# Performance work log

Measured on AMD Instinct MI355X. Metric: run time of the kernel, lower is better.

The kernel has to match this reference:

```python
import jax, jax.numpy as jnp
import numpy as np

BETA = 0.1
TRUNC = 1.0
MIN_VALID_RATIO = 0.3


def _wls_affine(x, y, w):
    # Weighted least squares fit of y ~ s*x + t over the last axis.
    sw = w.sum(-1)
    swx = (w * x).sum(-1)
    swy = (w * y).sum(-1)
    swxx = (w * x * x).sum(-1)
    swxy = (w * x * y).sum(-1)
    det = sw * swxx - swx * swx
    det = jnp.where(jnp.abs(det) < 1e-12, 1e-12, det)
    s = (sw * swxy - swx * swy) / det
    t = (swxx * swy - swx * swxy) / det
    return s, t


def _align_depth_affine(x, y, w, trunc):
    # Truncated robust affine alignment: initial WLS fit, then refit with
    # weights of points whose weighted residual exceeds `trunc` zeroed out
    # (falling back to the original weights if everything is truncated).
    s0, t0 = _wls_affine(x, y, w)
    e = w * jnp.abs(s0[..., None] * x + t0[..., None] - y)
    w2 = w * (e < trunc).astype(w.dtype)
    w2 = jnp.where(w2.sum(-1, keepdims=True) > 1e-8, w2, w)
    return _wls_affine(x, y, w2)


def _smooth(err, beta):
    if beta == 0:
        return err
    return jnp.where(err < beta, 0.5 * err * err / beta, err - 0.5 * beta)


def setup_inputs() -> dict:
    key = jax.random.key(0)
    k1, k2, k3 = jax.random.split(key, 3)
    B = 8
    P = 4096  # num_patches
    K = 256   # patch_pixel_count
    N = P * K
    pred_depth = jax.random.uniform(k1, (B, N), jnp.float32, 0.05, 5.0)
    gt_depth = jax.random.uniform(k2, (B, N), jnp.float32, 0.05, 5.0)
    mask = jax.random.bernoulli(k3, 0.8, (B, N))
    global_scale = jnp.ones((B,), jnp.float32)
    return {
        "pred_depth": pred_depth,
        "gt_depth": gt_depth,
        "mask": mask,
        "global_scale": global_scale,
        "num_patches": P,
        "patch_pixel_count": K,
    }


def reference(pred_depth, gt_depth, mask, global_scale, num_patches, patch_pixel_count):
    B = pred_depth.shape[0]
    P, K = num_patches, patch_pixel_count
    x = pred_depth.reshape(B, P, K)
    y = gt_depth.reshape(B, P, K)
    m = mask.reshape(B, P, K).astype(x.dtype)

    valid_ratio = m.mean(-1)                      # (B, P)
    msum = m.sum(-1)
    mean_depth = jnp.where(msum > 0, (y * m).sum(-1) / jnp.maximum(msum, 1.0), 1.0)

    w = m / jnp.maximum(y, 1e-5)                  # alignment weights (B, P, K)
    s, t = _align_depth_affine(x, y, w, TRUNC)    # (B, P) scale / shift per patch

    ratio = s / jnp.maximum(global_scale[:, None], 1e-12)
    gs_ok = jnp.where(global_scale[:, None] > 0, (ratio >= 0.1) & (ratio <= 10.0), True)
    valid = (valid_ratio >= MIN_VALID_RATIO) & (s > 0) & gs_ok  # (B, P)

    aligned = s[..., None] * x + t[..., None]
    pw = m / jnp.maximum(y, 0.1 * mean_depth[..., None])
    patch_loss = _smooth(jnp.abs(aligned - y) * pw, BETA).mean(-1)  # (B, P)

    vf = valid.astype(x.dtype)
    cnt = vf.sum()
    loss = jnp.where(cnt > 0, (patch_loss * vf).sum() / jnp.maximum(cnt, 1.0), 0.0)
    return loss
```

## Files before the change

### kernel.cpp

```cpp
#include <hip/hip_runtime.h>


#define WPB 4
#define NSLOTS 64
#define MAXBLK 2048

__device__ __forceinline__ float wredu(float v) {
#define DPP_ADD(ctrl)                                                        \
  v += __int_as_float(__builtin_amdgcn_update_dpp(                           \
      0, __float_as_int(v), (ctrl), 0xf, 0xf, true))
  DPP_ADD(0x111);
  DPP_ADD(0x112);
  DPP_ADD(0x114);
  DPP_ADD(0x118);
  DPP_ADD(0x142);
  DPP_ADD(0x143);
#undef DPP_ADD
  return __int_as_float(__builtin_amdgcn_readlane(__float_as_int(v), 63));
}

__device__ __forceinline__ float frcp(float x) {
  return __builtin_amdgcn_rcpf(x);
}

__global__ __launch_bounds__(256) void moge_patch_kernel(
    const float* __restrict__ xg,
    const float* __restrict__ yg,
    const int*   __restrict__ mg,
    const float* __restrict__ gsg,
    const int*   __restrict__ pP,
    const int*   __restrict__ pK,
    int B,
    float* __restrict__ ws,
    float* __restrict__ out) {
  const int P = pP[0];
  const int K = pK[0];
  const int lane = threadIdx.x & 63;
  const int wib  = threadIdx.x >> 6;
  const int total_patches = B * P;
  const int wave_stride = gridDim.x * WPB;
  const float invK = 1.0f / (float)K;

  if (K == 256) {
    int patch = blockIdx.x * WPB + wib;
    if (patch < total_patches) {
      const int loff = lane * 4;
      long base = (long)patch * 256 + loff;
      float4 x4 = *(const float4*)(xg + base);
      float4 y4 = *(const float4*)(yg + base);
      int4   m4 = *(const int4*)(mg + base);

      for (;;) {
        const int next = patch + wave_stride;
        const bool has_next = next < total_patches;
        const long nbase = (has_next ? (long)next * 256 : 0) + loff;
        const float4 nx4 = *(const float4*)(xg + nbase);
        const float4 ny4 = *(const float4*)(yg + nbase);
        const int4   nm4 = *(const int4*)(mg + nbase);

        float xr[4] = {x4.x, x4.y, x4.z, x4.w};
        float yr[4] = {y4.x, y4.y, y4.z, y4.w};
        float mr[4] = {m4.x ? 1.f : 0.f, m4.y ? 1.f : 0.f,
                       m4.z ? 1.f : 0.f, m4.w ? 1.f : 0.f};
        float wr[4];

        float sw = 0.f, swx = 0.f, swy = 0.f, swxx = 0.f, swxy = 0.f;
        float msum = 0.f, symsum = 0.f;
        #pragma unroll
        for (int i = 0; i < 4; ++i) {
          const float m = mr[i], xx = xr[i], yy = yr[i];
          const float w = m * frcp(fmaxf(yy, 1e-5f));
          wr[i] = w;
          const float wx = w * xx;
          sw += w; swx += wx; swy = fmaf(w, yy, swy);
          swxx = fmaf(wx, xx, swxx); swxy = fmaf(wx, yy, swxy);
          msum += m; symsum = fmaf(m, yy, symsum);
        }
        sw = wredu(sw); swx = wredu(swx); swy = wredu(swy);
        swxx = wredu(swxx); swxy = wredu(swxy);

        float det = sw * swxx - swx * swx;
        if (fabsf(det) < 1e-12f) det = 1e-12f;
        float rdet = frcp(det);
        const float s0 = (sw * swxy - swx * swy) * rdet;
        const float t0 = (swxx * swy - swx * swxy) * rdet;

        float sw2 = 0.f, swx2 = 0.f, swy2 = 0.f, swxx2 = 0.f, swxy2 = 0.f;
        #pragma unroll
        for (int i = 0; i < 4; ++i) {
          const float xx = xr[i], yy = yr[i], w = wr[i];
          const float e = w * fabsf(fmaf(s0, xx, t0) - yy);
          const float w2 = (e < 1.0f) ? w : 0.f;
          const float w2x = w2 * xx;
          sw2 += w2; swx2 += w2x; swy2 = fmaf(w2, yy, swy2);
          swxx2 = fmaf(w2x, xx, swxx2); swxy2 = fmaf(w2x, yy, swxy2);
        }
        sw2 = wredu(sw2); swx2 = wredu(swx2); swy2 = wredu(swy2);
        swxx2 = wredu(swxx2); swxy2 = wredu(swxy2);
        msum = wredu(msum); symsum = wredu(symsum);

        if (sw2 > 1e-8f) {
          sw = sw2; swx = swx2; swy = swy2; swxx = swxx2; swxy = swxy2;
        }
        det = sw * swxx - swx * swx;
        if (fabsf(det) < 1e-12f) det = 1e-12f;
        rdet = frcp(det);
        const float s = (sw * swxy - swx * swy) * rdet;
        const float t = (swxx * swy - swx * swxy) * rdet;

        const float mean_depth =
            (msum > 0.f) ? (symsum * frcp(fmaxf(msum, 1.f))) : 1.f;
        const float yfloor = 0.1f * mean_depth;

        float lsum = 0.f;
        #pragma unroll
        for (int i = 0; i < 4; ++i) {
          const float pw = mr[i] * frcp(fmaxf(yr[i], yfloor));
          const float err = fabsf(fmaf(s, xr[i], t) - yr[i]) * pw;
          lsum += (err < 0.1f) ? (5.0f * err * err) : (err - 0.05f);
        }
        const float patch_loss = wredu(lsum) * invK;

        const float gs = gsg[patch / P];
        const float ratio = s * frcp(fmaxf(gs, 1e-12f));
        const bool gs_ok = (gs > 0.f) ? (ratio >= 0.1f && ratio <= 10.0f) : true;
        const bool valid = (msum * invK >= 0.3f) && (s > 0.f) && gs_ok;

        if (lane == 0 && valid) {
          const int slot = patch & (NSLOTS - 1);
          atomicAdd(&ws[slot], patch_loss);
          atomicAdd(&ws[NSLOTS + slot], 1.0f);
        }

        if (!has_next) break;
        patch = next; x4 = nx4; y4 = ny4; m4 = nm4;
      }
    }
  } else {
    for (int patch = blockIdx.x * WPB + wib; patch < total_patches;
         patch += wave_stride) {
      const long base = (long)patch * (long)K;
      const float* xp = xg + base;
      const float* yp = yg + base;
      const int*   mp = mg + base;

      float sw = 0.f, swx = 0.f, swy = 0.f, swxx = 0.f, swxy = 0.f;
      float msum = 0.f, symsum = 0.f;
      for (int j = lane; j < K; j += 64) {
        const float m = mp[j] ? 1.f : 0.f;
        const float xx = xp[j], yy = yp[j];
        const float w = m * frcp(fmaxf(yy, 1e-5f));
        const float wx = w * xx;
        sw += w; swx += wx; swy = fmaf(w, yy, swy);
        swxx = fmaf(wx, xx, swxx); swxy = fmaf(wx, yy, swxy);
        msum += m; symsum = fmaf(m, yy, symsum);
      }
      sw = wredu(sw); swx = wredu(swx); swy = wredu(swy);
      swxx = wredu(swxx); swxy = wredu(swxy);
      msum = wredu(msum); symsum = wredu(symsum);

      float det = sw * swxx - swx * swx;
      if (fabsf(det) < 1e-12f) det = 1e-12f;
      float rdet = frcp(det);
      const float s0 = (sw * swxy - swx * swy) * rdet;
      const float t0 = (swxx * swy - swx * swxy) * rdet;

      float sw2 = 0.f, swx2 = 0.f, swy2 = 0.f, swxx2 = 0.f, swxy2 = 0.f;
      for (int j = lane; j < K; j += 64) {
        const float m = mp[j] ? 1.f : 0.f;
        const float xx = xp[j], yy = yp[j];
        const float w = m * frcp(fmaxf(yy, 1e-5f));
        const float e = w * fabsf(fmaf(s0, xx, t0) - yy);
        const float w2 = (e < 1.0f) ? w : 0.f;
        const float w2x = w2 * xx;
        sw2 += w2; swx2 += w2x; swy2 = fmaf(w2, yy, swy2);
        swxx2 = fmaf(w2x, xx, swxx2); swxy2 = fmaf(w2x, yy, swxy2);
      }
      sw2 = wredu(sw2); swx2 = wredu(swx2); swy2 = wredu(swy2);
      swxx2 = wredu(swxx2); swxy2 = wredu(swxy2);

      if (sw2 > 1e-8f) {
        sw = sw2; swx = swx2; swy = swy2; swxx = swxx2; swxy = swxy2;
      }
      det = sw * swxx - swx * swx;
      if (fabsf(det) < 1e-12f) det = 1e-12f;
      rdet = frcp(det);
      const float s = (sw * swxy - swx * swy) * rdet;
      const float t = (swxx * swy - swx * swxy) * rdet;

      const float mean_depth =
          (msum > 0.f) ? (symsum * frcp(fmaxf(msum, 1.f))) : 1.f;
      const float yfloor = 0.1f * mean_depth;

      float lsum = 0.f;
      for (int j = lane; j < K; j += 64) {
        const float m = mp[j] ? 1.f : 0.f;
        const float xx = xp[j], yy = yp[j];
        const float pw = m * frcp(fmaxf(yy, yfloor));
        const float err = fabsf(fmaf(s, xx, t) - yy) * pw;
        lsum += (err < 0.1f) ? (5.0f * err * err) : (err - 0.05f);
      }
      const float patch_loss = wredu(lsum) * invK;

      const float gs = gsg[patch / P];
      const float ratio = s * frcp(fmaxf(gs, 1e-12f));
      const bool gs_ok = (gs > 0.f) ? (ratio >= 0.1f && ratio <= 10.0f) : true;
      const bool valid = (msum * invK >= 0.3f) && (s > 0.f) && gs_ok;

      if (lane == 0 && valid) {
        const int slot = patch & (NSLOTS - 1);
        atomicAdd(&ws[slot], patch_loss);
        atomicAdd(&ws[NSLOTS + slot], 1.0f);
      }
    }
  }

  __syncthreads();
  __shared__ int is_last;
  if (threadIdx.x == 0) {
    unsigned int old = atomicAdd((unsigned int*)(ws + 2 * NSLOTS), 1u);
    is_last = (old == gridDim.x - 1) ? 1 : 0;
  }
  __syncthreads();
  if (is_last && threadIdx.x < 64) {
    __builtin_amdgcn_fence(__ATOMIC_ACQUIRE, "agent");
    float l = __hip_atomic_load(&ws[threadIdx.x], __ATOMIC_RELAXED,
                                __HIP_MEMORY_SCOPE_AGENT);
    float c = __hip_atomic_load(&ws[NSLOTS + threadIdx.x], __ATOMIC_RELAXED,
                                __HIP_MEMORY_SCOPE_AGENT);
    l = wredu(l);
    c = wredu(c);
    if (threadIdx.x == 0) out[0] = (c > 0.f) ? (l / fmaxf(c, 1.f)) : 0.f;
  }
}

extern "C" void kernel_launch(void* const* d_in, const int* in_sizes, int n_in,
                              void* d_out, int out_size, void* d_ws, size_t ws_size,
                              hipStream_t stream) {
  const float* pred = (const float*)d_in[0];
  const float* gt   = (const float*)d_in[1];
  const int*   mask = (const int*)d_in[2];
  const float* gs   = (const float*)d_in[3];
  const int*   pP   = (const int*)d_in[4];
  const int*   pK   = (const int*)d_in[5];
  const int B = in_sizes[3];
  const long total_pixels = (long)in_sizes[0];
  float* ws = (float*)d_ws;

  hipMemsetAsync(ws, 0, (2 * NSLOTS + 1) * sizeof(float), stream);

  long est_patches = total_pixels / 256;
  long blocks = (est_patches + WPB - 1) / WPB;
  if (blocks < 1) blocks = 1;
  if (blocks > MAXBLK) blocks = MAXBLK;
  moge_patch_kernel<<<(int)blocks, 256, 0, stream>>>(pred, gt, mask, gs, pP,
                                                     pK, B, ws, (float*)d_out);
}
```

Before: 144.1 us.

## Accumulate patch losses per block and finalize in a separate kernel

Each wave now accumulates valid patch losses and counts in registers, and the block combines them through shared memory before issuing one pair of atomics per block. The atomic slots are padded to 128-byte strides to reduce contention. The last-block detection with its counter atomic and acquire fence is replaced by a second tiny finalize kernel. This cuts global atomic traffic, but adds a second kernel launch on the stream.

```diff
diff --git a/kernel.cpp b/kernel.cpp
--- a/kernel.cpp
+++ b/kernel.cpp
@@ -31,8 +31,7 @@
     const int*   __restrict__ pP,
     const int*   __restrict__ pK,
     int B,
-    float* __restrict__ ws,
-    float* __restrict__ out) {
+    float* __restrict__ ws) {
   const int P = pP[0];
   const int K = pK[0];
   const int lane = threadIdx.x & 63;
@@ -40,6 +39,8 @@
   const int total_patches = B * P;
   const int wave_stride = gridDim.x * WPB;
   const float invK = 1.0f / (float)K;
+
+  float wloss = 0.f, wcnt = 0.f;
 
   if (K == 256) {
     int patch = blockIdx.x * WPB + wib;
@@ -126,11 +127,7 @@
         const bool gs_ok = (gs > 0.f) ? (ratio >= 0.1f && ratio <= 10.0f) : true;
         const bool valid = (msum * invK >= 0.3f) && (s > 0.f) && gs_ok;
 
-        if (lane == 0 && valid) {
-          const int slot = patch & (NSLOTS - 1);
-          atomicAdd(&ws[slot], patch_loss);
-          atomicAdd(&ws[NSLOTS + slot], 1.0f);
-        }
+        if (valid) { wloss += patch_loss; wcnt += 1.f; }
 
         if (!has_next) break;
         patch = next; x4 = nx4; y4 = ny4; m4 = nm4;
@@ -207,31 +204,29 @@
       const bool gs_ok = (gs > 0.f) ? (ratio >= 0.1f && ratio <= 10.0f) : true;
       const bool valid = (msum * invK >= 0.3f) && (s > 0.f) && gs_ok;
 
-      if (lane == 0 && valid) {
-        const int slot = patch & (NSLOTS - 1);
-        atomicAdd(&ws[slot], patch_loss);
-        atomicAdd(&ws[NSLOTS + slot], 1.0f);
-      }
+      if (valid) { wloss += patch_loss; wcnt += 1.f; }
     }
   }
 
+  __shared__ float sl[WPB], sc[WPB];
+  if (lane == 0) { sl[wib] = wloss; sc[wib] = wcnt; }
   __syncthreads();
-  __shared__ int is_last;
   if (threadIdx.x == 0) {
-    unsigned int old = atomicAdd((unsigned int*)(ws + 2 * NSLOTS), 1u);
-    is_last = (old == gridDim.x - 1) ? 1 : 0;
+    float bl = 0.f, bc = 0.f;
+    #pragma unroll
+    for (int i = 0; i < WPB; ++i) { bl += sl[i]; bc += sc[i]; }
+    const int slot = (blockIdx.x & (NSLOTS - 1)) * 32;
+    atomicAdd(&ws[slot], bl);
+    atomicAdd(&ws[slot + 1], bc);
   }
-  __syncthreads();
-  if (is_last && threadIdx.x < 64) {
-    __builtin_amdgcn_fence(__ATOMIC_ACQUIRE, "agent");
-    float l = __hip_atomic_load(&ws[threadIdx.x], __ATOMIC_RELAXED,
-                                __HIP_MEMORY_SCOPE_AGENT);
-    float c = __hip_atomic_load(&ws[NSLOTS + threadIdx.x], __ATOMIC_RELAXED,
-                                __HIP_MEMORY_SCOPE_AGENT);
-    l = wredu(l);
-    c = wredu(c);
-    if (threadIdx.x == 0) out[0] = (c > 0.f) ? (l / fmaxf(c, 1.f)) : 0.f;
-  }
+}
+
+__global__ void finalize_kernel(const float* __restrict__ ws,
+                                float* __restrict__ out) {
+  const int t = threadIdx.x;
+  float l = wredu(ws[t * 32]);
+  float c = wredu(ws[t * 32 + 1]);
+  if (t == 0) out[0] = (c > 0.f) ? (l / fmaxf(c, 1.f)) : 0.f;
 }
 
 extern "C" void kernel_launch(void* const* d_in, const int* in_sizes, int n_in,
@@ -247,12 +242,13 @@
   const long total_pixels = (long)in_sizes[0];
   float* ws = (float*)d_ws;
 
-  hipMemsetAsync(ws, 0, (2 * NSLOTS + 1) * sizeof(float), stream);
+  hipMemsetAsync(ws, 0, NSLOTS * 32 * sizeof(float), stream);
 
   long est_patches = total_pixels / 256;
   long blocks = (est_patches + WPB - 1) / WPB;
   if (blocks < 1) blocks = 1;
   if (blocks > MAXBLK) blocks = MAXBLK;
   moge_patch_kernel<<<(int)blocks, 256, 0, stream>>>(pred, gt, mask, gs, pP,
-                                                     pK, B, ws, (float*)d_out);
-}
+                                                     pK, B, ws);
+  finalize_kernel<<<1, 64, 0, stream>>>(ws, (float*)d_out);
+}
```

New measurement: 128.9 us. -10.5%, faster.
